# Kernel tuning notes

Hardware: AMD Instinct MI355X
Metric: run time of the kernel (lower is better)

## Reference

```python
import jax, jax.numpy as jnp
import numpy as np

V, FN, CIN, HID, PTS = 50000, 100000, 3, 256, 10000
TEMP = 0.1
EPS = 1e-20


def line_mesh_graph(f, Vn):
    # f: [F,3] int triangles. Build the 'line mesh': one node per unique mesh edge.
    fe = jnp.concatenate([f[:, :2], f[:, 1:], f[:, jnp.array([2, 0])]], 0)  # [3F,2]
    fe = jnp.sort(fe, axis=1)
    keys = fe[:, 0] * Vn + fe[:, 1]                       # [3F] unique key per undirected edge
    ukeys, inv = jnp.unique(keys, return_inverse=True)
    edge_node = jnp.stack([ukeys // Vn, ukeys % Vn], -1)  # [E,2] endpoints of each edge-node
    E = ukeys.shape[0]
    feid = inv.reshape(3, -1).T                           # [F,3] edge-node id per face edge
    # line-graph connectivity: edges of the same face are mutual neighbors, plus self-loops
    srcs, dsts = [], []
    for i, j in ((0, 1), (1, 0), (1, 2), (2, 1), (2, 0), (0, 2)):
        srcs.append(feid[:, i]); dsts.append(feid[:, j])
    loop = jnp.arange(E)
    edge = jnp.stack([jnp.concatenate(srcs + [loop]), jnp.concatenate(dsts + [loop])], 0)  # [2,NE]
    return edge, edge_node, keys


def gsn_conv(x, edge, Ws, Wn, b):
    # GSNConv stand-in: self transform + mean-aggregated neighbor transform
    s, d = edge[0], edge[1]
    N = x.shape[0]
    deg = jax.ops.segment_sum(jnp.ones_like(s, x.dtype), d, num_segments=N)
    agg = jax.ops.segment_sum(x[s], d, num_segments=N) / jnp.clip(deg, 1.0)[:, None]
    return x @ Ws + agg @ Wn + b


def gumbel_mask(logits, temperature, num, key):
    U = jax.random.uniform(key, logits.shape)
    g = -jnp.log(-jnp.log(U + EPS) + EPS)
    y = jax.nn.softmax((logits + g) / temperature, -1)[:, 0]  # [E]
    _, ind = jax.lax.top_k(y, num)
    y_hard = jnp.zeros_like(y).at[ind].set(1.0)
    mask = jax.lax.stop_gradient(y_hard - y) + y              # straight-through one-hot
    return mask, y_hard == 1.0


def mesh_collapse(f, keys, pool_edge, Vn):
    # Vectorized replacement of the per-pool-edge python loop: hash-join pooled edge keys
    # against all 3F face-edge keys via sorted search.
    PE = pool_edge.shape[0]
    pool_idx = jnp.arange(Vn, Vn + PE)
    edge_keys = keys.reshape(3, -1).T                     # [F,3] (cols: e01,e12,e20)
    pk = pool_edge[:, 0] * Vn + pool_edge[:, 1]
    order = jnp.argsort(pk); pks = pk[order]
    flat = edge_keys.reshape(-1)
    pos = jnp.clip(jnp.searchsorted(pks, flat), 0, PE - 1)
    found = pks[pos] == flat
    pei = jnp.where(found, pool_idx[order[pos]], -1).reshape(-1, 3)  # pool_edge_idx [F,3]
    fm = found.reshape(-1, 3)
    pen = fm.sum(1)                                       # pool_edge_num per face
    psi = (fm * jnp.arange(3)).sum(1)                     # pool_start_idx per face
    vv = jnp.stack([f[:, 0], pei[:, 0], f[:, 1], pei[:, 1], f[:, 2], pei[:, 2]], -1)
    nf0 = f[pen == 0]
    fv1 = vv[pen == 1]; s1 = psi[pen == 1]
    fv1 = jnp.concatenate([fv1[s1 == 0], jnp.roll(fv1[s1 == 1], -2, 1), jnp.roll(fv1[s1 == 2], 2, 1)], 0)
    nf1 = jnp.concatenate([jnp.stack([fv1[:, 0], fv1[:, 1], fv1[:, 4]], -1),
                           jnp.stack([fv1[:, 1], fv1[:, 2], fv1[:, 4]], -1)], 0)
    fv2 = vv[pen == 2]; s2 = psi[pen == 2]
    fv2 = jnp.concatenate([fv2[s2 == 1], jnp.roll(fv2[s2 == 2], 2, 1), jnp.roll(fv2[s2 == 3], -2, 1)], 0)
    nf2 = jnp.concatenate([jnp.stack([fv2[:, 0], fv2[:, 1], fv2[:, 4]], -1),
                           jnp.stack([fv2[:, 1], fv2[:, 2], fv2[:, 3]], -1),
                           jnp.stack([fv2[:, 1], fv2[:, 3], fv2[:, 4]], -1)], 0)
    fv3 = vv[pen == 3]
    nf3 = jnp.concatenate([jnp.stack([fv3[:, 0], fv3[:, 1], fv3[:, 5]], -1),
                           jnp.stack([fv3[:, 1], fv3[:, 2], fv3[:, 3]], -1),
                           jnp.stack([fv3[:, 1], fv3[:, 3], fv3[:, 5]], -1),
                           jnp.stack([fv3[:, 3], fv3[:, 4], fv3[:, 5]], -1)], 0)
    new_faces = jnp.concatenate([nf0, nf1, nf2, nf3], 0)
    ne = jnp.concatenate([new_faces[:, :2], new_faces[:, 1:], new_faces[:, jnp.array([2, 0])]], 0)
    ai = jnp.arange(Vn + PE)
    ne = jnp.concatenate([jnp.stack([ai, ai], -1), ne], 0)
    return new_faces, ne.T


def setup_inputs():
    key = jax.random.key(0)
    ks = jax.random.split(key, 10)
    s1 = 1.0 / np.sqrt(CIN); s2 = 1.0 / np.sqrt(HID)
    return {
        'input': jax.random.normal(ks[0], (1, V, CIN), jnp.float32),
        'face': jax.random.randint(ks[1], (1, FN, 3), 0, V),
        'coord': jax.random.normal(ks[2], (1, V, 3), jnp.float32),
        'detail_points': jax.random.normal(ks[3], (1, PTS, 3), jnp.float32),
        'div': 5,
        'W1s': jax.random.normal(ks[4], (CIN, HID), jnp.float32) * s1,
        'W1n': jax.random.normal(ks[5], (CIN, HID), jnp.float32) * s1,
        'b1': jnp.zeros((HID,), jnp.float32),
        'W2s': jax.random.normal(ks[6], (HID, 2), jnp.float32) * s2,
        'W2n': jax.random.normal(ks[7], (HID, 2), jnp.float32) * s2,
        'b2': jnp.zeros((2,), jnp.float32),
    }


def reference(input, face, coord, detail_points, div, W1s, W1n, b1, W2s, W2n, b2):
    # B=1 (data-dependent per-sample output sizes make batch stacking only valid then)
    x0, f = input[0], face[0]
    Vn = x0.shape[0]
    edge, edge_node, keys = line_mesh_graph(f, Vn)
    xe = 0.5 * (x0[edge_node[:, 0]] + x0[edge_node[:, 1]])   # edge-node features [E,C]
    h = jax.nn.relu(gsn_conv(xe, edge, W1s, W1n, b1))
    out = jax.nn.sigmoid(gsn_conv(h, edge, W2s, W2n, b2))    # [E,2]
    mask, pool_ind = gumbel_mask(out, TEMP, out.shape[0] // div, jax.random.key(42))
    pool_edge = edge_node[pool_ind]                          # [PE,2]
    new_faces, new_edges = mesh_collapse(f, keys, pool_edge, Vn)
    return edge_node[None], new_faces[None], new_edges[None], mask[None]
```

## Files before the change

### kernel.cpp

```cpp
#include <hip/hip_runtime.h>
#include <stdint.h>

typedef uint32_t u32;
typedef uint64_t u64;

#define VN 50000
#define FN 100000
#define K3F 300000
#define EMAX 300000
#define NB1 1172
#define NBC 98
#define NBH 293
#define NBS 293

#define W_KPA    0u
#define W_KPB    600000u
#define W_RANKU  1200000u
#define W_SEGOFF 1500000u
#define W_FEID   1800004u
#define W_XE     2100004u
#define W_PK     3000004u
#define W_P      3100004u
#define W_Q      3700004u
#define W_Y      4300004u
#define W_YMAP   4600004u
#define W_T64    4900004u
#define W_SEL    5500068u
#define W_SELR   5800068u
#define W_CAT    6100068u
#define W_CATR   6200068u
#define W_NFI    6300068u
#define W_HIST   7500068u
#define W_SUMS   7800100u
#define W_CATH   7804196u
#define W_TKH    7805220u
#define W_DONE   7805476u
#define W_SCAL   7805504u

#define S_E 0
#define S_NUM 1
#define S_PFX 2
#define S_KREM 3
#define S_TU 4
#define S_R 5
#define S_NF 6
#define S_NEN 7
#define S_O1 8
#define S_O2 9
#define S_O3 10
#define S_RS 16
#define S_GS 24
#define S_GP 32

__device__ __forceinline__ void tf2x32(u32 x0, u32 x1, u32& o0, u32& o1) {
  const u32 ks0 = 0u, ks1 = 42u, ks2 = 0x1BD11BDAu ^ 0u ^ 42u;
  x0 += ks0; x1 += ks1;
#define TFR(r) { x0 += x1; x1 = (x1<<(r))|(x1>>(32-(r))); x1 ^= x0; }
  TFR(13) TFR(15) TFR(26) TFR(6)   x0 += ks1; x1 += ks2 + 1u;
  TFR(17) TFR(29) TFR(16) TFR(24)  x0 += ks2; x1 += ks0 + 2u;
  TFR(13) TFR(15) TFR(26) TFR(6)   x0 += ks0; x1 += ks1 + 3u;
  TFR(17) TFR(29) TFR(16) TFR(24)  x0 += ks1; x1 += ks2 + 4u;
  TFR(13) TFR(15) TFR(26) TFR(6)   x0 += ks2; x1 += ks0 + 5u;
#undef TFR
  o0 = x0; o1 = x1;
}

__global__ void scan_blocks(const u32* __restrict__ in, u32* __restrict__ out,
                            u32* __restrict__ sums, int n) {
  __shared__ u32 lds[256];
  int t = threadIdx.x;
  int base = blockIdx.x*1024 + t*4;
  u32 v[4]; u32 tot = 0;
  for (int k = 0; k < 4; ++k) { v[k] = (base+k < n) ? in[base+k] : 0u; tot += v[k]; }
  lds[t] = tot; __syncthreads();
  for (int o = 1; o < 256; o <<= 1) {
    u32 x = (t >= o) ? lds[t-o] : 0u; __syncthreads();
    lds[t] += x; __syncthreads();
  }
  u32 excl = lds[t] - tot;
  if (t == 255) sums[blockIdx.x] = lds[255];
  u32 run = excl;
  for (int k = 0; k < 4; ++k) { if (base+k < n) out[base+k] = run; run += v[k]; }
}

__global__ void scan_flagblocks(const u64* __restrict__ kp, u32* __restrict__ out,
                                u32* __restrict__ sums, int n) {
  __shared__ u32 lds[256];
  int t = threadIdx.x;
  int base = blockIdx.x*1024 + t*4;
  u32 v[4]; u32 tot = 0;
  for (int k = 0; k < 4; ++k) {
    int i = base + k;
    u32 f = 0;
    if (i < n) f = (i == 0 || (u32)(kp[i-1]>>32) != (u32)(kp[i]>>32)) ? 1u : 0u;
    v[k] = f; tot += f;
  }
  lds[t] = tot; __syncthreads();
  for (int o = 1; o < 256; o <<= 1) {
    u32 x = (t >= o) ? lds[t-o] : 0u; __syncthreads();
    lds[t] += x; __syncthreads();
  }
  u32 excl = lds[t] - tot;
  if (t == 255) sums[blockIdx.x] = lds[255];
  u32 run = excl;
  for (int k = 0; k < 4; ++k) { if (base+k < n) out[base+k] = run; run += v[k]; }
}

__global__ void scan_sums(u32* __restrict__ s, int nb) {
  __shared__ u32 lds[256];
  __shared__ u32 carry;
  int t = threadIdx.x;
  if (t == 0) carry = 0;
  __syncthreads();
  for (int base = 0; base < nb; base += 1024) {
    int idx = base + t*4;
    u32 v[4]; u32 tot = 0;
    for (int k = 0; k < 4; ++k) { v[k] = (idx+k < nb) ? s[idx+k] : 0u; tot += v[k]; }
    lds[t] = tot; __syncthreads();
    for (int o = 1; o < 256; o <<= 1) {
      u32 x = (t >= o) ? lds[t-o] : 0u; __syncthreads();
      lds[t] += x; __syncthreads();
    }
    u32 excl = lds[t] - tot;
    u32 ctot = lds[255];
    u32 c = carry;
    __syncthreads();
    u32 run = c + excl;
    for (int k = 0; k < 4; ++k) { if (idx+k < nb) s[idx+k] = run; run += v[k]; }
    if (t == 0) carry = c + ctot;
    __syncthreads();
  }
}

__global__ void scan64_src(const u32* __restrict__ ymap, const u32* __restrict__ scal,
                           u64* __restrict__ part, u64* __restrict__ sums) {
  __shared__ u64 lds[256];
  int t = threadIdx.x;
  int base = blockIdx.x*1024 + t*4;
  int E = (int)scal[S_E];
  u32 TU = scal[S_TU];
  u64 v[4]; u64 tot = 0;
  for (int k = 0; k < 4; ++k) {
    int e = base + k;
    u64 val = 0;
    if (e < E) {
      u32 u = ymap[e];
      if (u > TU) val = 1ull;
      else if (u == TU) val = 1ull << 32;
    }
    v[k] = val; tot += val;
  }
  lds[t] = tot; __syncthreads();
  for (int o = 1; o < 256; o <<= 1) {
    u64 x = (t >= o) ? lds[t-o] : 0ull; __syncthreads();
    lds[t] += x; __syncthreads();
  }
  u64 excl = lds[t] - tot;
  if (t == 255) sums[blockIdx.x] = lds[255];
  u64 run = excl;
  for (int k = 0; k < 4; ++k) { part[base+k] = run; run += v[k]; }
}

__global__ void scan64_sums(u64* __restrict__ s, int nb) {
  __shared__ u64 lds[256];
  int t = threadIdx.x;
  int idx = t*4;
  u64 v[4]; u64 tot = 0;
  for (int k = 0; k < 4; ++k) { v[k] = (idx+k < nb) ? s[idx+k] : 0ull; tot += v[k]; }
  lds[t] = tot; __syncthreads();
  for (int o = 1; o < 256; o <<= 1) {
    u64 x = (t >= o) ? lds[t-o] : 0ull; __syncthreads();
    lds[t] += x; __syncthreads();
  }
  u64 excl = lds[t] - tot;
  u64 run = excl;
  for (int k = 0; k < 4; ++k) { if (idx+k < nb) s[idx+k] = run; run += v[k]; }
}

__global__ void k_sel2(const u32* __restrict__ ymap, const u64* __restrict__ part,
                       const u64* __restrict__ sums, const u32* __restrict__ scal,
                       u32* __restrict__ sel, u32* __restrict__ selr) {
  int e = blockIdx.x*256 + threadIdx.x;
  if (e >= EMAX) return;
  int E = (int)scal[S_E];
  u32 TU = scal[S_TU], R = scal[S_R];
  u64 pre = part[e] + sums[e>>10];
  u32 GTpre = (u32)pre, TIEpre = (u32)(pre >> 32);
  u32 v = 0;
  if (e < E) {
    u32 u = ymap[e];
    v = (u > TU) || (u == TU && TIEpre < R);
  }
  sel[e] = v ? 1u : 0u;
  selr[e] = GTpre + min(TIEpre, R);
}

__global__ void k_rhist(const u64* __restrict__ kp, u32* __restrict__ hist,
                        int shift, int nb) {
  __shared__ u32 h[256];
  int t = threadIdx.x;
  h[t] = 0; __syncthreads();
  int i = blockIdx.x*256 + t;
  if (i < K3F) atomicAdd(&h[((u32)(kp[i]>>32) >> shift) & 255u], 1u);
  __syncthreads();
  hist[(u32)t*nb + blockIdx.x] = h[t];
}

__global__ void k_rscat(const u64* __restrict__ kp, u64* __restrict__ okp,
                        const u32* __restrict__ hist, const u32* __restrict__ sums,
                        int shift, int nb) {
  __shared__ u64 ball[4][8];
  __shared__ u64 vmask[4];
  int t = threadIdx.x, w = t>>6, lane = t&63;
  int i = blockIdx.x*256 + t;
  bool valid = i < K3F;
  u64 v = valid ? kp[i] : 0ull;
  u32 d = ((u32)(v>>32) >> shift) & 255u;
  for (int bit = 0; bit < 8; ++bit) {
    u64 bm = __ballot(valid && ((d>>bit)&1u));
    if (lane == 0) ball[w][bit] = bm;
  }
  u64 vb = __ballot(valid ? 1 : 0);
  if (lane == 0) vmask[w] = vb;
  __syncthreads();
  if (valid) {
    u32 rank = 0;
    for (int ww = 0; ww < w; ++ww) {
      u64 m = vmask[ww];
      for (int bit = 0; bit < 8; ++bit) { u64 bb = ball[ww][bit]; m &= ((d>>bit)&1u) ? bb : ~bb; }
      rank += (u32)__popcll(m);
    }
    u64 m = vmask[w];
    for (int bit = 0; bit < 8; ++bit) { u64 bb = ball[w][bit]; m &= ((d>>bit)&1u) ? bb : ~bb; }
    rank += (u32)__popcll(m & ((1ull<<lane)-1ull));
    u32 h = d*(u32)nb + blockIdx.x;
    u32 pos = hist[h] + sums[h>>10] + rank;
    okp[pos] = v;
  }
}

__global__ void k_keys(const int* __restrict__ face,
                       const float* __restrict__ W1s, const float* __restrict__ W1n,
                       const float* __restrict__ b1,
                       const float* __restrict__ W2s, const float* __restrict__ W2n,
                       float* __restrict__ pk,
                       u64* __restrict__ kp, u32* __restrict__ hist,
                       u32* __restrict__ tkh, u32* __restrict__ done) {
  __shared__ u32 h[256];
  int t = threadIdx.x;
  h[t] = 0;
  __syncthreads();
  if (blockIdx.x == 0) {
    tkh[t] = 0u;
    if (t < 16) done[t] = 0u;
    float* p = pk + t*12;
    p[0] = W1s[t]; p[1] = W1s[256+t]; p[2] = W1s[512+t];
    p[3] = W1n[t]; p[4] = W1n[256+t]; p[5] = W1n[512+t];
    p[6] = b1[t];
    p[7] = W2s[2*t]; p[8] = W2s[2*t+1];
    p[9] = W2n[2*t]; p[10] = W2n[2*t+1];
    p[11] = 0.0f;
  }
  int i = blockIdx.x*256 + t;
  if (i < K3F) {
    int s = i / FN, f = i - s*FN;
    int v0 = face[f*3 + s];
    int v1 = face[f*3 + (s == 2 ? 0 : s+1)];
    int a = min(v0, v1), b = max(v0, v1);
    u32 key = ((u32)a * (u32)VN + (u32)b) ^ 0x80000000u;
    kp[i] = ((u64)key << 32) | (u32)i;
    atomicAdd(&h[key & 255u], 1u);
  }
  __syncthreads();
  hist[(u32)t*NB1 + blockIdx.x] = h[t];
}

__global__ void k_uwrite(const u64* __restrict__ kp, const u32* __restrict__ rankp,
                         const u32* __restrict__ sums, const float* __restrict__ x,
                         u32* __restrict__ segoff, u32* __restrict__ feid,
                         float* __restrict__ xe, float* __restrict__ dout,
                         u32* __restrict__ scal, const int* __restrict__ divp) {
  int p = blockIdx.x*256 + threadIdx.x;
  if (p >= K3F) return;
  u64 v = kp[p];
  u32 cur = (u32)(v >> 32);
  u32 fl = (p == 0 || (u32)(kp[p-1] >> 32) != cur) ? 1u : 0u;
  u32 rk = rankp[p] + sums[p>>10];
  if (fl) {
    u32 e = rk;
    segoff[e] = (u32)p;
    int k = (int)(cur ^ 0x80000000u);
    long long kk = (long long)k;
    long long qq = (kk - (kk < 0 ? (long long)(VN-1) : 0ll)) / VN;
    int q = (int)qq;
    int r = (int)(kk - qq * VN);
    dout[2*e]   = (float)q;
    dout[2*e+1] = (float)r;
    u32 i0 = (u32)(q < 0 ? q + VN : q);
    u32 i1 = (u32)r;
    for (int c = 0; c < 3; ++c) xe[e*3+c] = 0.5f*(x[i0*3+c] + x[i1*3+c]);
  }
  u32 id = rk - 1u + fl;
  u32 i = (u32)v;
  u32 s = i / FN, f = i - s*FN;
  feid[f*3 + s] = id;
  if (p == K3F-1) {
    u32 E = rk + fl;
    u32 num = E / (u32)divp[0];
    scal[S_E] = E; scal[S_NUM] = num;
    segoff[E] = (u32)K3F;
    scal[S_PFX] = 0u; scal[S_KREM] = num;
  }
}

__device__ __forceinline__ void agg_neighbors(int e, u32 st, u32 en,
                                              const u64* __restrict__ kp,
                                              const u32* __restrict__ feid,
                                              const float* __restrict__ v, int stride,
                                              float* acc0, float* acc1, float* acc2) {
  const int sslot[6] = {0,1,1,2,2,0};
  const int dslot[6] = {1,0,2,1,0,2};
  float c0 = 0.f, c1 = 0.f, c2 = 0.f;
  for (int b = 0; b < 6; ++b) {
    int j = dslot[b], isl = sslot[b];
    for (u32 p = st; p < en; ++p) {
      u32 i = (u32)kp[p];
      u32 s = i / FN;
      if ((int)s == j) {
        u32 f = i - s*FN;
        u32 u = feid[f*3 + isl];
        c0 += v[u*stride]; c1 += v[u*stride+1]; if (stride == 3) c2 += v[u*stride+2];
      }
    }
  }
  c0 += v[e*stride]; c1 += v[e*stride+1]; if (stride == 3) c2 += v[e*stride+2];
  *acc0 = c0; *acc1 = c1; *acc2 = c2;
}

__global__ void k_l12(const float* __restrict__ xe, const u32* __restrict__ segoff,
                      const u64* __restrict__ kp, const u32* __restrict__ feid,
                      const u32* __restrict__ scal, const float* __restrict__ pk,
                      float* __restrict__ P, float* __restrict__ Q) {
  int e = blockIdx.x*256 + threadIdx.x;
  if (e >= (int)scal[S_E]) return;
  u32 st = segoff[e], en = segoff[e+1];
  float c0, c1, c2;
  agg_neighbors(e, st, en, kp, feid, xe, 3, &c0, &c1, &c2);
  float x0 = xe[e*3], x1 = xe[e*3+1], x2 = xe[e*3+2];
  float dg = (float)(2u*(en - st) + 1u);
  float m0 = c0/dg, m1 = c1/dg, m2 = c2/dg;
  float p0 = 0.f, p1 = 0.f, q0 = 0.f, q1 = 0.f;
#pragma unroll 8
  for (int hh = 0; hh < 256; ++hh) {
    const float* w = pk + hh*12;
    float s1 = x0*w[0] + x1*w[1] + x2*w[2];
    float s2 = m0*w[3] + m1*w[4] + m2*w[5];
    float h = fmaxf(s1 + s2 + w[6], 0.0f);
    p0 += h*w[7];  p1 += h*w[8];
    q0 += h*w[9];  q1 += h*w[10];
  }
  P[2*e] = p0; P[2*e+1] = p1; Q[2*e] = q0; Q[2*e+1] = q1;
}

__global__ void k_scores(const float* __restrict__ P, const float* __restrict__ Q,
                         const u32* __restrict__ segoff, const u64* __restrict__ kp,
                         const u32* __restrict__ feid,
                         const float* __restrict__ b2, const u32* __restrict__ scal,
                         float* __restrict__ Y, u32* __restrict__ ymap) {
  int e = blockIdx.x*256 + threadIdx.x;
  u32 E = scal[S_E];
  if (e >= (int)E) return;
  u32 st = segoff[e], en = segoff[e+1];
  float a0, a1, dummy;
  agg_neighbors(e, st, en, kp, feid, Q, 2, &a0, &a1, &dummy);
  float dg = (float)(2u*(en - st) + 1u);
  float z0 = P[2*e]   + a0/dg + b2[0];
  float z1 = P[2*e+1] + a1/dg + b2[1];
  float l0 = 1.0f/(1.0f + expf(-z0));
  float l1 = 1.0f/(1.0f + expf(-z1));
  u32 g0b, g1b;
  { u32 o0,o1; tf2x32(0u, 2u*(u32)e,      o0, o1); g0b = o0 ^ o1; }
  { u32 o0,o1; tf2x32(0u, 2u*(u32)e + 1u, o0, o1); g1b = o0 ^ o1; }
  float U0 = __uint_as_float((g0b>>9) | 0x3f800000u) - 1.0f;
  float U1 = __uint_as_float((g1b>>9) | 0x3f800000u) - 1.0f;
  float g0 = -logf(-logf(U0 + 1e-20f) + 1e-20f);
  float g1 = -logf(-logf(U1 + 1e-20f) + 1e-20f);
  float A0 = (l0 + g0)/0.1f;
  float A1 = (l1 + g1)/0.1f;
  float mx = fmaxf(A0, A1);
  float e0 = expf(A0-mx), e1 = expf(A1-mx);
  float y = e0/(e0+e1);
  Y[e] = y;
  ymap[e] = __float_as_uint(y) | 0x80000000u;
}

__global__ void k_tkround(const u32* __restrict__ ymap, u32* __restrict__ scal,
                          u32* __restrict__ hist, u32* __restrict__ done, int byte) {
  __shared__ u32 h[256];
  __shared__ u32 s2[256];
  __shared__ u32 chosen_s;
  __shared__ u32 lastflag;
  int t = threadIdx.x;
  h[t] = 0u;
  if (t == 0) lastflag = 0u;
  __syncthreads();
  int E = (int)scal[S_E];
  u32 pfx = scal[S_PFX];
  int base = blockIdx.x*1024;
  for (int k = 0; k < 4; ++k) {
    int e = base + k*256 + t;
    if (e < E) {
      u32 u = ymap[e];
      bool match = (byte == 3) || ((u >> ((byte+1)*8)) == pfx);
      if (match) atomicAdd(&h[(u >> (byte*8)) & 255u], 1u);
    }
  }
  __syncthreads();
  u32 c = h[t];
  if (c) atomicAdd(&hist[t], c);
  __syncthreads();
  if (t == 0) {
    __threadfence();
    u32 old = atomicAdd(&done[byte], 1u);
    if (old == gridDim.x - 1u) lastflag = 1u;
  }
  __syncthreads();
  if (!lastflag) return;
  __threadfence();
  u32 v = atomicExch(&hist[t], 0u);
  s2[t] = v;
  if (t == 0) chosen_s = 0u;
  __syncthreads();
  for (int o = 1; o < 256; o <<= 1) {
    u32 x = (t + o < 256) ? s2[t+o] : 0u; __syncthreads();
    s2[t] += x; __syncthreads();
  }
  u32 krem = scal[S_KREM];
  if (s2[t] >= krem) atomicMax(&chosen_s, (u32)t);
  __syncthreads();
  if (t == 0) {
    u32 chosen = chosen_s;
    u32 sufnext = (chosen < 255u) ? s2[chosen+1] : 0u;
    u32 newkrem = krem - sufnext;
    u32 npfx = (scal[S_PFX] << 8) | chosen;
    scal[S_PFX] = npfx; scal[S_KREM] = newkrem;
    if (byte == 0) { scal[S_TU] = npfx; scal[S_R] = newkrem; }
  }
}

__global__ void k_catfused(const u32* __restrict__ feid, const u32* __restrict__ sel,
                           u32* __restrict__ cat, u32* __restrict__ ch) {
  __shared__ u32 h[8];
  int t = threadIdx.x;
  if (t < 8) h[t] = 0u;
  __syncthreads();
  int base = blockIdx.x*1024 + t*4;
  for (int k = 0; k < 4; ++k) {
    int f = base + k;
    if (f < FN) {
      u32 m0 = sel[feid[f*3]], m1 = sel[feid[f*3+1]], m2 = sel[feid[f*3+2]];
      u32 pen = m0 + m1 + m2;
      u32 psi = m1 + 2u*m2;
      u32 c = (pen == 0) ? 0u : (pen == 1) ? (1u+psi) : (pen == 2) ? (3u+psi) : 7u;
      cat[f] = c;
      atomicAdd(&h[c], 1u);
    }
  }
  __syncthreads();
  if (t < 8) ch[(u32)t*NBC + blockIdx.x] = h[t];
}

__global__ void k_catoff(u32* __restrict__ ch, u32* __restrict__ scal) {
  __shared__ u32 lds[256];
  __shared__ u32 ex[1024];
  int t = threadIdx.x;
  u32 v[4]; u32 tot = 0;
  for (int k = 0; k < 4; ++k) {
    int i = t*4 + k;
    u32 x = (i < 8*NBC) ? ch[i] : 0u;
    v[k] = x; tot += x;
  }
  lds[t] = tot; __syncthreads();
  for (int o = 1; o < 256; o <<= 1) {
    u32 x = (t >= o) ? lds[t-o] : 0u; __syncthreads();
    lds[t] += x; __syncthreads();
  }
  u32 excl = lds[t] - tot;
  u32 run = excl;
  for (int k = 0; k < 4; ++k) { ex[t*4+k] = run; run += v[k]; }
  __syncthreads();
  for (int k = 0; k < 4; ++k) {
    int i = t*4 + k;
    if (i < 8*NBC) ch[i] = ex[i];
  }
  if (t == 0) {
    u32 total = lds[255];
    u32 bnd[9];
    for (int c = 0; c < 8; ++c) bnd[c] = ex[c*NBC];
    bnd[8] = total;
    u32 tot8[8];
    for (int c = 0; c < 8; ++c) tot8[c] = bnd[c+1] - bnd[c];
    u32 n0 = tot8[0], n1 = tot8[1]+tot8[2]+tot8[3], n2 = tot8[4]+tot8[5]+tot8[6], n3 = tot8[7];
    u32 NF = n0 + 2u*n1 + 3u*n2 + 4u*n3;
    u32 E = scal[S_E], num = scal[S_NUM];
    u32 NEn = (u32)VN + num + 3u*NF;
    scal[S_NF] = NF; scal[S_NEN] = NEn;
    scal[S_O1] = 2u*E;
    scal[S_O2] = 2u*E + 3u*NF;
    scal[S_O3] = 2u*E + 3u*NF + 2u*NEn;
    u32 RS[8] = {0u, n0,n0,n0, n0+2u*n1, n0+2u*n1, n0+2u*n1, n0+2u*n1+3u*n2};
    u32 GS[8] = {0u, n1,n1,n1, n2,n2,n2, n3};
    u32 GP[8] = {0u, n0,n0,n0, n0+n1, n0+n1, n0+n1, n0+n1+n2};
    for (int i = 0; i < 8; ++i) { scal[S_RS+i] = RS[i]; scal[S_GS+i] = GS[i]; scal[S_GP+i] = GP[i]; }
  }
}

__global__ void k_catrank(const u32* __restrict__ cat, const u32* __restrict__ ch,
                          u32* __restrict__ cr) {
  __shared__ u32 lds[256];
  int t = threadIdx.x;
  int base = blockIdx.x*1024 + t*4;
  u32 cc[4], loc[4];
  u32 cnt[8] = {0,0,0,0,0,0,0,0};
  for (int k = 0; k < 4; ++k) {
    int i = base + k;
    if (i < FN) { u32 c = cat[i]; cc[k] = c; loc[k] = cnt[c]++; }
    else cc[k] = 8u;
  }
  u32 tb[8];
  for (int c = 0; c < 8; ++c) {
    lds[t] = cnt[c]; __syncthreads();
    for (int o = 1; o < 256; o <<= 1) {
      u32 x = (t >= o) ? lds[t-o] : 0u; __syncthreads();
      lds[t] += x; __syncthreads();
    }
    tb[c] = lds[t] - cnt[c];
    __syncthreads();
  }
  for (int k = 0; k < 4; ++k) {
    int i = base + k;
    if (i < FN) { u32 c = cc[k]; cr[i] = ch[c*NBC + blockIdx.x] + tb[c] + loc[k]; }
  }
}

__global__ void k_wfaces(const int* __restrict__ face, const u32* __restrict__ cat,
                         const u32* __restrict__ cr, const u32* __restrict__ feid,
                         const u32* __restrict__ selr, const u32* __restrict__ scal,
                         int* __restrict__ nfi, float* __restrict__ dout) {
  int f = blockIdx.x*256 + threadIdx.x;
  if (f >= FN) return;
  const int nfc[8] = {1,2,2,2,3,3,3,4};
  const int tri[8][4][3] = {
    {{0,2,4},{0,0,0},{0,0,0},{0,0,0}},
    {{0,1,4},{1,2,4},{0,0,0},{0,0,0}},
    {{2,3,0},{3,4,0},{0,0,0},{0,0,0}},
    {{4,5,2},{5,0,2},{0,0,0},{0,0,0}},
    {{0,1,4},{1,2,3},{1,3,4},{0,0,0}},
    {{4,5,2},{5,0,1},{5,1,2},{0,0,0}},
    {{2,3,0},{3,4,5},{3,5,0},{0,0,0}},
    {{0,1,5},{1,2,3},{1,3,5},{3,4,5}}};
  u32 c = cat[f];
  int cv[6];
  cv[0] = face[f*3];   cv[2] = face[f*3+1]; cv[4] = face[f*3+2];
  cv[1] = VN + (int)selr[feid[f*3]];
  cv[3] = VN + (int)selr[feid[f*3+1]];
  cv[5] = VN + (int)selr[feid[f*3+2]];
  u32 g  = cr[f] - scal[S_GP + c];
  u32 o1 = scal[S_O1];
  for (int j = 0; j < nfc[c]; ++j) {
    u32 row = scal[S_RS + c] + (u32)j*scal[S_GS + c] + g;
    for (int m = 0; m < 3; ++m) {
      int v = cv[tri[c][j][m]];
      nfi[row*3 + m] = v;
      dout[o1 + row*3 + m] = (float)v;
    }
  }
}

__global__ void k_wne(const int* __restrict__ nfi, const u32* __restrict__ scal,
                      float* __restrict__ dout) {
  int i = blockIdx.x*256 + threadIdx.x;
  u32 NEn = scal[S_NEN];
  if (i >= (int)NEn) return;
  u32 NF = scal[S_NF];
  u32 Vp = (u32)VN + scal[S_NUM];
  u32 o2 = scal[S_O2];
  int a, b;
  if ((u32)i < Vp) { a = i; b = i; }
  else {
    u32 j = (u32)i - Vp;
    u32 blk = j / NF, r = j - blk*NF;
    int i0 = (blk == 0) ? 0 : (blk == 1) ? 1 : 2;
    int i1 = (blk == 0) ? 1 : (blk == 1) ? 2 : 0;
    a = nfi[r*3 + i0]; b = nfi[r*3 + i1];
  }
  dout[o2 + i] = (float)a;
  dout[o2 + NEn + i] = (float)b;
}

__global__ void k_wmask(const u32* __restrict__ sel, const float* __restrict__ Y,
                        const u32* __restrict__ scal, float* __restrict__ dout) {
  int e = blockIdx.x*256 + threadIdx.x;
  if (e >= (int)scal[S_E]) return;
  float y = Y[e];
  float yh = sel[e] ? 1.0f : 0.0f;
  dout[scal[S_O3] + e] = (yh - y) + y;
}

static void radix_pass(u32* hist, u32* sums, u64* kin, u64* kout, int shift,
                       bool do_hist, hipStream_t st) {
  if (do_hist) k_rhist<<<NB1, 256, 0, st>>>(kin, hist, shift, NB1);
  scan_blocks<<<NBS, 256, 0, st>>>(hist, hist, sums, NB1*256);
  scan_sums<<<1, 256, 0, st>>>(sums, NBS);
  k_rscat<<<NB1, 256, 0, st>>>(kin, kout, hist, sums, shift, NB1);
}

extern "C" void kernel_launch(void* const* d_in, const int* in_sizes, int n_in,
                              void* d_out, int out_size, void* d_ws, size_t ws_size,
                              hipStream_t stream) {
  const float* x    = (const float*)d_in[0];
  const int*   face = (const int*)d_in[1];
  const int*   divp = (const int*)d_in[4];
  const float* W1s  = (const float*)d_in[5];
  const float* W1n  = (const float*)d_in[6];
  const float* b1   = (const float*)d_in[7];
  const float* W2s  = (const float*)d_in[8];
  const float* W2n  = (const float*)d_in[9];
  const float* b2   = (const float*)d_in[10];
  float* out = (float*)d_out;
  u32* W = (u32*)d_ws;

  u64 *KPA = (u64*)(W+W_KPA), *KPB = (u64*)(W+W_KPB);
  u32 *RK = W+W_RANKU;
  u32 *HIST = W+W_HIST, *SUMS = W+W_SUMS, *SCAL = W+W_SCAL;
  u32 *TKH = W+W_TKH, *DONE = W+W_DONE;
  u64 *T64 = (u64*)(W+W_T64);
  u64 *SUMS64 = (u64*)(W+W_SUMS);

  k_keys<<<NB1, 256, 0, stream>>>(face, W1s, W1n, b1, W2s, W2n, (float*)(W+W_PK),
                                  KPA, HIST, TKH, DONE);
  radix_pass(HIST, SUMS, KPA, KPB,  0, false, stream);
  radix_pass(HIST, SUMS, KPB, KPA,  8, true,  stream);
  radix_pass(HIST, SUMS, KPA, KPB, 16, true,  stream);
  radix_pass(HIST, SUMS, KPB, KPA, 24, true,  stream);
  scan_flagblocks<<<NBS, 256, 0, stream>>>(KPA, RK, SUMS, K3F);
  scan_sums<<<1, 256, 0, stream>>>(SUMS, NBS);
  k_uwrite<<<NB1, 256, 0, stream>>>(KPA, RK, SUMS, x, W+W_SEGOFF, W+W_FEID,
                                    (float*)(W+W_XE), out, SCAL, divp);

  k_l12<<<NB1, 256, 0, stream>>>((float*)(W+W_XE), W+W_SEGOFF, KPA, W+W_FEID, SCAL,
                                 (float*)(W+W_PK), (float*)(W+W_P), (float*)(W+W_Q));
  k_scores<<<NB1, 256, 0, stream>>>((float*)(W+W_P), (float*)(W+W_Q), W+W_SEGOFF, KPA,
                                    W+W_FEID, b2, SCAL, (float*)(W+W_Y), W+W_YMAP);

  for (int byte = 3; byte >= 0; --byte)
    k_tkround<<<NBH, 256, 0, stream>>>(W+W_YMAP, SCAL, TKH, DONE, byte);
  scan64_src<<<NBS, 256, 0, stream>>>(W+W_YMAP, SCAL, T64, SUMS64);
  scan64_sums<<<1, 256, 0, stream>>>(SUMS64, NBS);
  k_sel2<<<NB1, 256, 0, stream>>>(W+W_YMAP, T64, SUMS64, SCAL, W+W_SEL, W+W_SELR);

  k_catfused<<<NBC, 256, 0, stream>>>(W+W_FEID, W+W_SEL, W+W_CAT, W+W_CATH);
  k_catoff<<<1, 256, 0, stream>>>(W+W_CATH, SCAL);
  k_catrank<<<NBC, 256, 0, stream>>>(W+W_CAT, W+W_CATH, W+W_CATR);
  k_wfaces<<<391, 256, 0, stream>>>(face, W+W_CAT, W+W_CATR, W+W_FEID, W+W_SELR, SCAL,
                                    (int*)(W+W_NFI), out);
  k_wne<<<5118, 256, 0, stream>>>((int*)(W+W_NFI), SCAL, out);
  k_wmask<<<NB1, 256, 0, stream>>>(W+W_SEL, (float*)(W+W_Y), SCAL, out);
}
```

Before: 320.0 us.

## Fuse radix histogram into scatter and process two edges per thread

```diff
diff --git a/kernel.cpp b/kernel.cpp
--- a/kernel.cpp
+++ b/kernel.cpp
@@ -9,33 +9,35 @@
 #define K3F 300000
 #define EMAX 300000
 #define NB1 1172
+#define NBS 293
+#define NBH 293
 #define NBC 98
-#define NBH 293
-#define NBS 293
+#define HALF1 150016
+#define NBL 586
 
 #define W_KPA    0u
 #define W_KPB    600000u
-#define W_RANKU  1200000u
-#define W_SEGOFF 1500000u
-#define W_FEID   1800004u
-#define W_XE     2100004u
-#define W_PK     3000004u
-#define W_P      3100004u
-#define W_Q      3700004u
-#define W_Y      4300004u
-#define W_YMAP   4600004u
-#define W_T64    4900004u
-#define W_SEL    5500068u
-#define W_SELR   5800068u
-#define W_CAT    6100068u
-#define W_CATR   6200068u
-#define W_NFI    6300068u
-#define W_HIST   7500068u
-#define W_SUMS   7800100u
-#define W_CATH   7804196u
-#define W_TKH    7805220u
-#define W_DONE   7805476u
-#define W_SCAL   7805504u
+#define W_SEGOFF 1200000u
+#define W_FEID   1500004u
+#define W_XE     1800004u
+#define W_PK     2700004u
+#define W_P      2703076u
+#define W_Q      3303076u
+#define W_Y      3903076u
+#define W_YMAP   4203076u
+#define W_T64    4503076u
+#define W_SEL    5103140u
+#define W_SELR   5403140u
+#define W_CAT    5703140u
+#define W_CATR   5803140u
+#define W_NFI    5903140u
+#define W_HIST   7103140u
+#define W_HIST2  7403172u
+#define W_SUMS   7703204u
+#define W_CATH   7707300u
+#define W_TKH    7708324u
+#define W_DONE   7708580u
+#define W_SCAL   7708612u
 
 #define S_E 0
 #define S_NUM 1
@@ -66,7 +68,7 @@
 }
 
 __global__ void scan_blocks(const u32* __restrict__ in, u32* __restrict__ out,
-                            u32* __restrict__ sums, int n) {
+                            u32* __restrict__ sums, int n, u32* __restrict__ zeronext) {
   __shared__ u32 lds[256];
   int t = threadIdx.x;
   int base = blockIdx.x*1024 + t*4;
@@ -80,7 +82,13 @@
   u32 excl = lds[t] - tot;
   if (t == 255) sums[blockIdx.x] = lds[255];
   u32 run = excl;
-  for (int k = 0; k < 4; ++k) { if (base+k < n) out[base+k] = run; run += v[k]; }
+  for (int k = 0; k < 4; ++k) {
+    if (base+k < n) {
+      out[base+k] = run;
+      if (zeronext) zeronext[base+k] = 0u;
+    }
+    run += v[k];
+  }
 }
 
 __global__ void scan_flagblocks(const u64* __restrict__ kp, u32* __restrict__ out,
@@ -195,20 +203,9 @@
   selr[e] = GTpre + min(TIEpre, R);
 }
 
-__global__ void k_rhist(const u64* __restrict__ kp, u32* __restrict__ hist,
-                        int shift, int nb) {
-  __shared__ u32 h[256];
-  int t = threadIdx.x;
-  h[t] = 0; __syncthreads();
-  int i = blockIdx.x*256 + t;
-  if (i < K3F) atomicAdd(&h[((u32)(kp[i]>>32) >> shift) & 255u], 1u);
-  __syncthreads();
-  hist[(u32)t*nb + blockIdx.x] = h[t];
-}
-
 __global__ void k_rscat(const u64* __restrict__ kp, u64* __restrict__ okp,
                         const u32* __restrict__ hist, const u32* __restrict__ sums,
-                        int shift, int nb) {
+                        int shift, int nb, u32* __restrict__ histnext) {
   __shared__ u64 ball[4][8];
   __shared__ u64 vmask[4];
   int t = threadIdx.x, w = t>>6, lane = t&63;
@@ -236,6 +233,10 @@
     u32 h = d*(u32)nb + blockIdx.x;
     u32 pos = hist[h] + sums[h>>10] + rank;
     okp[pos] = v;
+    if (histnext) {
+      u32 d2 = ((u32)(v>>32) >> (shift+8)) & 255u;
+      atomicAdd(&histnext[d2*(u32)nb + (pos>>8)], 1u);
+    }
   }
 }
 
@@ -252,7 +253,7 @@
   __syncthreads();
   if (blockIdx.x == 0) {
     tkh[t] = 0u;
-    if (t < 16) done[t] = 0u;
+    if (t < 32) done[t] = 0u;
     float* p = pk + t*12;
     p[0] = W1s[t]; p[1] = W1s[256+t]; p[2] = W1s[512+t];
     p[3] = W1n[t]; p[4] = W1n[256+t]; p[5] = W1n[512+t];
@@ -341,41 +342,50 @@
                       const u64* __restrict__ kp, const u32* __restrict__ feid,
                       const u32* __restrict__ scal, const float* __restrict__ pk,
                       float* __restrict__ P, float* __restrict__ Q) {
-  int e = blockIdx.x*256 + threadIdx.x;
-  if (e >= (int)scal[S_E]) return;
-  u32 st = segoff[e], en = segoff[e+1];
-  float c0, c1, c2;
-  agg_neighbors(e, st, en, kp, feid, xe, 3, &c0, &c1, &c2);
-  float x0 = xe[e*3], x1 = xe[e*3+1], x2 = xe[e*3+2];
-  float dg = (float)(2u*(en - st) + 1u);
-  float m0 = c0/dg, m1 = c1/dg, m2 = c2/dg;
-  float p0 = 0.f, p1 = 0.f, q0 = 0.f, q1 = 0.f;
-#pragma unroll 8
+  int e1 = blockIdx.x*256 + threadIdx.x;
+  int E = (int)scal[S_E];
+  if (e1 >= E) return;
+  int e2 = e1 + HALF1;
+  bool v2 = e2 < E;
+  int e2c = v2 ? e2 : e1;
+  u32 st1 = segoff[e1], en1 = segoff[e1+1];
+  u32 st2 = segoff[e2c], en2 = segoff[e2c+1];
+  float c0a,c1a,c2a, c0b,c1b,c2b;
+  agg_neighbors(e1,  st1, en1, kp, feid, xe, 3, &c0a,&c1a,&c2a);
+  agg_neighbors(e2c, st2, en2, kp, feid, xe, 3, &c0b,&c1b,&c2b);
+  float x0a=xe[e1*3],  x1a=xe[e1*3+1],  x2a=xe[e1*3+2];
+  float x0b=xe[e2c*3], x1b=xe[e2c*3+1], x2b=xe[e2c*3+2];
+  float dga = (float)(2u*(en1-st1)+1u), dgb = (float)(2u*(en2-st2)+1u);
+  float m0a=c0a/dga, m1a=c1a/dga, m2a=c2a/dga;
+  float m0b=c0b/dgb, m1b=c1b/dgb, m2b=c2b/dgb;
+  float p0a=0,p1a=0,q0a=0,q1a=0, p0b=0,p1b=0,q0b=0,q1b=0;
+#pragma unroll 4
   for (int hh = 0; hh < 256; ++hh) {
     const float* w = pk + hh*12;
-    float s1 = x0*w[0] + x1*w[1] + x2*w[2];
-    float s2 = m0*w[3] + m1*w[4] + m2*w[5];
-    float h = fmaxf(s1 + s2 + w[6], 0.0f);
-    p0 += h*w[7];  p1 += h*w[8];
-    q0 += h*w[9];  q1 += h*w[10];
-  }
-  P[2*e] = p0; P[2*e+1] = p1; Q[2*e] = q0; Q[2*e+1] = q1;
-}
-
-__global__ void k_scores(const float* __restrict__ P, const float* __restrict__ Q,
-                         const u32* __restrict__ segoff, const u64* __restrict__ kp,
-                         const u32* __restrict__ feid,
-                         const float* __restrict__ b2, const u32* __restrict__ scal,
-                         float* __restrict__ Y, u32* __restrict__ ymap) {
-  int e = blockIdx.x*256 + threadIdx.x;
-  u32 E = scal[S_E];
-  if (e >= (int)E) return;
+    float w0=w[0],w1=w[1],w2=w[2],w3=w[3],w4=w[4],w5=w[5],w6=w[6];
+    float w7=w[7],w8=w[8],w9=w[9],w10=w[10];
+    float s1a = x0a*w0 + x1a*w1 + x2a*w2;
+    float s2a = m0a*w3 + m1a*w4 + m2a*w5;
+    float ha = fmaxf(s1a + s2a + w6, 0.0f);
+    p0a += ha*w7;  p1a += ha*w8;  q0a += ha*w9;  q1a += ha*w10;
+    float s1b = x0b*w0 + x1b*w1 + x2b*w2;
+    float s2b = m0b*w3 + m1b*w4 + m2b*w5;
+    float hb = fmaxf(s1b + s2b + w6, 0.0f);
+    p0b += hb*w7;  p1b += hb*w8;  q0b += hb*w9;  q1b += hb*w10;
+  }
+  P[2*e1] = p0a; P[2*e1+1] = p1a; Q[2*e1] = q0a; Q[2*e1+1] = q1a;
+  if (v2) { P[2*e2] = p0b; P[2*e2+1] = p1b; Q[2*e2] = q0b; Q[2*e2+1] = q1b; }
+}
+
+__device__ __forceinline__ void score_one(int e, const float* P, const float* Q,
+                                          const u32* segoff, const u64* kp, const u32* feid,
+                                          float b20, float b21, float* yo, u32* ymo) {
   u32 st = segoff[e], en = segoff[e+1];
   float a0, a1, dummy;
   agg_neighbors(e, st, en, kp, feid, Q, 2, &a0, &a1, &dummy);
   float dg = (float)(2u*(en - st) + 1u);
-  float z0 = P[2*e]   + a0/dg + b2[0];
-  float z1 = P[2*e+1] + a1/dg + b2[1];
+  float z0 = P[2*e]   + a0/dg + b20;
+  float z1 = P[2*e+1] + a1/dg + b21;
   float l0 = 1.0f/(1.0f + expf(-z0));
   float l1 = 1.0f/(1.0f + expf(-z1));
   u32 g0b, g1b;
@@ -388,10 +398,29 @@
   float A0 = (l0 + g0)/0.1f;
   float A1 = (l1 + g1)/0.1f;
   float mx = fmaxf(A0, A1);
-  float e0 = expf(A0-mx), e1 = expf(A1-mx);
-  float y = e0/(e0+e1);
-  Y[e] = y;
-  ymap[e] = __float_as_uint(y) | 0x80000000u;
+  float e0 = expf(A0-mx), e1v = expf(A1-mx);
+  float y = e0/(e0+e1v);
+  *yo = y;
+  *ymo = __float_as_uint(y) | 0x80000000u;
+}
+
+__global__ void k_scores(const float* __restrict__ P, const float* __restrict__ Q,
+                         const u32* __restrict__ segoff, const u64* __restrict__ kp,
+                         const u32* __restrict__ feid,
+                         const float* __restrict__ b2, const u32* __restrict__ scal,
+                         float* __restrict__ Y, u32* __restrict__ ymap) {
+  int e1 = blockIdx.x*256 + threadIdx.x;
+  int E = (int)scal[S_E];
+  if (e1 >= E) return;
+  int e2 = e1 + HALF1;
+  bool v2 = e2 < E;
+  int e2c = v2 ? e2 : e1;
+  float b20 = b2[0], b21 = b2[1];
+  float ya, yb; u32 ma, mb;
+  score_one(e1,  P, Q, segoff, kp, feid, b20, b21, &ya, &ma);
+  score_one(e2c, P, Q, segoff, kp, feid, b20, b21, &yb, &mb);
+  Y[e1] = ya; ymap[e1] = ma;
+  if (v2) { Y[e2] = yb; ymap[e2] = mb; }
 }
 
 __global__ void k_tkround(const u32* __restrict__ ymap, u32* __restrict__ scal,
@@ -607,12 +636,11 @@
   dout[scal[S_O3] + e] = (yh - y) + y;
 }
 
-static void radix_pass(u32* hist, u32* sums, u64* kin, u64* kout, int shift,
-                       bool do_hist, hipStream_t st) {
-  if (do_hist) k_rhist<<<NB1, 256, 0, st>>>(kin, hist, shift, NB1);
-  scan_blocks<<<NBS, 256, 0, st>>>(hist, hist, sums, NB1*256);
+static void radix_pass(u32* hist, u32* histnext, u32* sums, u64* kin, u64* kout,
+                       int shift, hipStream_t st) {
+  scan_blocks<<<NBS, 256, 0, st>>>(hist, hist, sums, NB1*256, histnext);
   scan_sums<<<1, 256, 0, st>>>(sums, NBS);
-  k_rscat<<<NB1, 256, 0, st>>>(kin, kout, hist, sums, shift, NB1);
+  k_rscat<<<NB1, 256, 0, st>>>(kin, kout, hist, sums, shift, NB1, histnext);
 }
 
 extern "C" void kernel_launch(void* const* d_in, const int* in_sizes, int n_in,
@@ -631,26 +659,26 @@
   u32* W = (u32*)d_ws;
 
   u64 *KPA = (u64*)(W+W_KPA), *KPB = (u64*)(W+W_KPB);
-  u32 *RK = W+W_RANKU;
-  u32 *HIST = W+W_HIST, *SUMS = W+W_SUMS, *SCAL = W+W_SCAL;
+  u32 *HIST = W+W_HIST, *HIST2 = W+W_HIST2, *SUMS = W+W_SUMS, *SCAL = W+W_SCAL;
   u32 *TKH = W+W_TKH, *DONE = W+W_DONE;
+  u32 *RK = W+W_T64;
   u64 *T64 = (u64*)(W+W_T64);
   u64 *SUMS64 = (u64*)(W+W_SUMS);
 
   k_keys<<<NB1, 256, 0, stream>>>(face, W1s, W1n, b1, W2s, W2n, (float*)(W+W_PK),
                                   KPA, HIST, TKH, DONE);
-  radix_pass(HIST, SUMS, KPA, KPB,  0, false, stream);
-  radix_pass(HIST, SUMS, KPB, KPA,  8, true,  stream);
-  radix_pass(HIST, SUMS, KPA, KPB, 16, true,  stream);
-  radix_pass(HIST, SUMS, KPB, KPA, 24, true,  stream);
+  radix_pass(HIST,  HIST2,   SUMS, KPA, KPB,  0, stream);
+  radix_pass(HIST2, HIST,    SUMS, KPB, KPA,  8, stream);
+  radix_pass(HIST,  HIST2,   SUMS, KPA, KPB, 16, stream);
+  radix_pass(HIST2, nullptr, SUMS, KPB, KPA, 24, stream);
   scan_flagblocks<<<NBS, 256, 0, stream>>>(KPA, RK, SUMS, K3F);
   scan_sums<<<1, 256, 0, stream>>>(SUMS, NBS);
   k_uwrite<<<NB1, 256, 0, stream>>>(KPA, RK, SUMS, x, W+W_SEGOFF, W+W_FEID,
                                     (float*)(W+W_XE), out, SCAL, divp);
 
-  k_l12<<<NB1, 256, 0, stream>>>((float*)(W+W_XE), W+W_SEGOFF, KPA, W+W_FEID, SCAL,
+  k_l12<<<NBL, 256, 0, stream>>>((float*)(W+W_XE), W+W_SEGOFF, KPA, W+W_FEID, SCAL,
                                  (float*)(W+W_PK), (float*)(W+W_P), (float*)(W+W_Q));
-  k_scores<<<NB1, 256, 0, stream>>>((float*)(W+W_P), (float*)(W+W_Q), W+W_SEGOFF, KPA,
+  k_scores<<<NBL, 256, 0, stream>>>((float*)(W+W_P), (float*)(W+W_Q), W+W_SEGOFF, KPA,
                                     W+W_FEID, b2, SCAL, (float*)(W+W_Y), W+W_YMAP);
 
   for (int byte = 3; byte >= 0; --byte)
```

New measurement: 343.7 us. +7.4%, slower.
